# Optimization experiments

Measured on AMD Instinct MI355X. Metric: run time of the kernel, lower is better.

The kernel has to match this reference:

```python
import jax, jax.numpy as jnp
import numpy as np

N, D, NUM_CLASSES = 4096, 1024, 10


def setup_inputs() -> dict:
    key = jax.random.key(0)
    k1, k2, k3 = jax.random.split(key, 3)
    return {
        "fm_s": jax.random.normal(k1, (N, D), dtype=jnp.float32),
        "fm_t": jax.random.normal(k2, (N, D), dtype=jnp.float32),
        "targets": jax.random.randint(k3, (N,), 0, NUM_CLASSES, dtype=jnp.int64),
        "fusion_true": 0,
    }


def reference(fm_s, fm_t, targets, fusion_true):
    # fusion_true == False branch of CL.forward (multi_index unused).
    # Pairwise squared distances ||s_i - t_j||^2 via the GEMM expansion
    # instead of materializing the [N, N, D] difference tensor.
    s2 = jnp.sum(fm_s * fm_s, axis=-1)            # [N]
    t2 = jnp.sum(fm_t * fm_t, axis=-1)            # [N]
    cross = jnp.einsum('id,jd->ij', fm_s, fm_t)   # [N, N]
    d2 = s2[:, None] + t2[None, :] - 2.0 * cross  # [N, N]

    # self_mask_pos[i, j] = 1 where targets[i] == targets[j]
    mask_pos = (targets[:, None] == targets[None, :]).astype(d2.dtype)  # [N, N]
    row_norm = jnp.sum(mask_pos, axis=-1, keepdims=True)                # [N, 1], >= 1

    loss_pos = d2 * mask_pos / row_norm           # [N, N]
    return jnp.mean(jnp.sum(loss_pos, axis=-1))   # scalar
```

## Files before the change

kernel.cpp:

```cpp
#include <hip/hip_runtime.h>

#define N_ROWS 4096
#define D_DIM  1024
#define NCLS   10

#define NSLICE     4
#define SLICE_W    (D_DIM / NSLICE)
#define CHUNK_ROWS 64
#define NCHUNK     (N_ROWS / CHUNK_ROWS)
#define NB2        (NCHUNK * NSLICE)
#define NB3        512

#define OFF_MEAN 0
#define OFF_PL   (NCLS * D_DIM)
#define OFF_PT2  (OFF_PL + NB3)
#define OFF_PT   (OFF_PT2 + NB2)
#define DET_FLOATS (OFF_PT + NCHUNK * NCLS * D_DIM)
#define ATOMIC_FLOATS OFF_PT

__global__ void k_partialT(const float* __restrict__ fm_t,
                           const int* __restrict__ tgt,
                           float* __restrict__ partialT,
                           float* __restrict__ pt2) {
    int chunk = blockIdx.x / NSLICE;
    int slice = blockIdx.x % NSLICE;
    int tid   = threadIdx.x;

    __shared__ int tl[CHUNK_ROWS];
    if (tid < CHUNK_ROWS) tl[tid] = tgt[chunk * CHUNK_ROWS + tid];
    __syncthreads();

    float acc[NCLS];
#pragma unroll
    for (int k = 0; k < NCLS; ++k) acc[k] = 0.f;
    float acc2 = 0.f;

    int col = slice * SLICE_W + tid;
    const float* base = fm_t + (size_t)chunk * CHUNK_ROWS * D_DIM + col;
#pragma unroll 4
    for (int r = 0; r < CHUNK_ROWS; ++r) {
        float v = base[(size_t)r * D_DIM];
        int   c = tl[r];
        acc2 += v * v;
#pragma unroll
        for (int k = 0; k < NCLS; ++k) acc[k] += (c == k) ? v : 0.f;
    }

    float* out = partialT + (size_t)chunk * NCLS * D_DIM + col;
#pragma unroll
    for (int k = 0; k < NCLS; ++k) out[k * D_DIM] = acc[k];

    __shared__ float red[256];
    red[tid] = acc2;
    __syncthreads();
    for (int s = 128; s > 0; s >>= 1) {
        if (tid < s) red[tid] += red[tid + s];
        __syncthreads();
    }
    if (tid == 0) pt2[blockIdx.x] = red[0];
}

__global__ void k_reduceT(const float* __restrict__ partialT,
                          const int* __restrict__ tgt,
                          float* __restrict__ meanT) {
    int tid = threadIdx.x;

    __shared__ int hist[NCLS];
    if (tid < NCLS) hist[tid] = 0;
    __syncthreads();
    for (int i = tid; i < N_ROWS; i += 256) atomicAdd(&hist[tgt[i]], 1);
    __syncthreads();

    int cell = blockIdx.x * 256 + tid;
    if (cell >= NCLS * D_DIM) return;
    float s = 0.f;
#pragma unroll 8
    for (int k = 0; k < NCHUNK; ++k)
        s += partialT[(size_t)k * NCLS * D_DIM + cell];
    meanT[cell] = s / (float)hist[cell / D_DIM];
}

__global__ void k_zero(float* __restrict__ p, int n) {
    int i = blockIdx.x * blockDim.x + threadIdx.x;
    if (i < n) p[i] = 0.f;
}

__global__ void k_partialT_atomic(const float* __restrict__ fm_t,
                                  const int* __restrict__ tgt,
                                  float* __restrict__ sumT,
                                  float* __restrict__ pt2) {
    int chunk = blockIdx.x / NSLICE;
    int slice = blockIdx.x % NSLICE;
    int tid   = threadIdx.x;

    __shared__ int tl[CHUNK_ROWS];
    if (tid < CHUNK_ROWS) tl[tid] = tgt[chunk * CHUNK_ROWS + tid];
    __syncthreads();

    float acc[NCLS];
#pragma unroll
    for (int k = 0; k < NCLS; ++k) acc[k] = 0.f;
    float acc2 = 0.f;

    int col = slice * SLICE_W + tid;
    const float* base = fm_t + (size_t)chunk * CHUNK_ROWS * D_DIM + col;
    for (int r = 0; r < CHUNK_ROWS; ++r) {
        float v = base[(size_t)r * D_DIM];
        int   c = tl[r];
        acc2 += v * v;
#pragma unroll
        for (int k = 0; k < NCLS; ++k) acc[k] += (c == k) ? v : 0.f;
    }
#pragma unroll
    for (int k = 0; k < NCLS; ++k) atomicAdd(&sumT[k * D_DIM + col], acc[k]);

    __shared__ float red[256];
    red[tid] = acc2;
    __syncthreads();
    for (int s = 128; s > 0; s >>= 1) {
        if (tid < s) red[tid] += red[tid + s];
        __syncthreads();
    }
    if (tid == 0) pt2[blockIdx.x] = red[0];
}

__global__ void k_divmean(float* __restrict__ meanT, const int* __restrict__ tgt) {
    int tid = threadIdx.x;
    __shared__ int hist[NCLS];
    if (tid < NCLS) hist[tid] = 0;
    __syncthreads();
    for (int i = tid; i < N_ROWS; i += 256) atomicAdd(&hist[tgt[i]], 1);
    __syncthreads();
    int cell = blockIdx.x * 256 + tid;
    if (cell >= NCLS * D_DIM) return;
    meanT[cell] = meanT[cell] / (float)hist[cell / D_DIM];
}

__global__ void k_main(const float* __restrict__ fm_s,
                       const int* __restrict__ tgt,
                       const float* __restrict__ meanT,
                       float* __restrict__ partialLoss) {
    int tid = threadIdx.x;
    int bid = blockIdx.x;
    float acc = 0.f;

    const int ROWS_PER_BLK = N_ROWS / NB3;
#pragma unroll
    for (int r = 0; r < ROWS_PER_BLK; ++r) {
        int row = bid * ROWS_PER_BLK + r;
        int c   = tgt[row];
        const float4* s4 = (const float4*)(fm_s + (size_t)row * D_DIM);
        const float4* m4 = (const float4*)(meanT + (size_t)c * D_DIM);
        float4 sv = s4[tid];
        float4 mv = m4[tid];
        acc += sv.x * sv.x + sv.y * sv.y + sv.z * sv.z + sv.w * sv.w
             - 2.f * (sv.x * mv.x + sv.y * mv.y + sv.z * mv.z + sv.w * mv.w);
    }

    __shared__ float red[256];
    red[tid] = acc;
    __syncthreads();
    for (int s = 128; s > 0; s >>= 1) {
        if (tid < s) red[tid] += red[tid + s];
        __syncthreads();
    }
    if (tid == 0) partialLoss[bid] = red[0];
}

__global__ void k_final(const float* __restrict__ partialLoss,
                        const float* __restrict__ pt2,
                        float* __restrict__ out) {
    int tid = threadIdx.x;
    double acc = 0.0;
    for (int i = tid; i < NB3; i += 256) acc += (double)partialLoss[i];
    acc += (double)pt2[tid];
    __shared__ double red[256];
    red[tid] = acc;
    __syncthreads();
    for (int s = 128; s > 0; s >>= 1) {
        if (tid < s) red[tid] += red[tid + s];
        __syncthreads();
    }
    if (tid == 0) out[0] = (float)(red[0] / (double)N_ROWS);
}

extern "C" void kernel_launch(void* const* d_in, const int* in_sizes, int n_in,
                              void* d_out, int out_size, void* d_ws, size_t ws_size,
                              hipStream_t stream) {
    const float* fm_s = (const float*)d_in[0];
    const float* fm_t = (const float*)d_in[1];
    const int*   tgt  = (const int*)d_in[2];

    float* ws       = (float*)d_ws;
    float* meanT    = ws + OFF_MEAN;
    float* ploss    = ws + OFF_PL;
    float* pt2      = ws + OFF_PT2;
    float* partialT = ws + OFF_PT;
    float* outp     = (float*)d_out;

    if (ws_size >= (size_t)DET_FLOATS * sizeof(float)) {
        k_partialT<<<NB2, 256, 0, stream>>>(fm_t, tgt, partialT, pt2);
        k_reduceT<<<(NCLS * D_DIM + 255) / 256, 256, 0, stream>>>(partialT, tgt, meanT);
    } else {
        k_zero<<<(NCLS * D_DIM + 255) / 256, 256, 0, stream>>>(meanT, NCLS * D_DIM);
        k_partialT_atomic<<<NB2, 256, 0, stream>>>(fm_t, tgt, meanT, pt2);
        k_divmean<<<(NCLS * D_DIM + 255) / 256, 256, 0, stream>>>(meanT, tgt);
    }

    k_main<<<NB3, 256, 0, stream>>>(fm_s, tgt, meanT, ploss);
    k_final<<<1, 256, 0, stream>>>(ploss, pt2, outp);
}
```

Measured before the change: 28.92 us.

## Compute loss from per-class sums of both matrices in two kernels

Restructures the computation so that both fm_s and fm_t are reduced into per-class column sums in a single pass, and the cross term becomes a dot product of the class sums divided by class counts. The per-row k_main pass over fm_s and the separate final kernel are removed. A last-block atomic counter in pass 2 performs the final reduction, cutting the launch count from four to two. The change adds a larger partial-sum workspace and a threadfence/counter protocol, and class dispatch uses a wave-uniform switch via readfirstlane.

```diff
diff --git a/kernel.cpp b/kernel.cpp
--- a/kernel.cpp
+++ b/kernel.cpp
@@ -4,51 +4,80 @@
 #define D_DIM  1024
 #define NCLS   10
 
-#define NSLICE     4
-#define SLICE_W    (D_DIM / NSLICE)
-#define CHUNK_ROWS 64
-#define NCHUNK     (N_ROWS / CHUNK_ROWS)
-#define NB2        (NCHUNK * NSLICE)
-#define NB3        512
-
-#define OFF_MEAN 0
-#define OFF_PL   (NCLS * D_DIM)
-#define OFF_PT2  (OFF_PL + NB3)
-#define OFF_PT   (OFF_PT2 + NB2)
-#define DET_FLOATS (OFF_PT + NCHUNK * NCLS * D_DIM)
-#define ATOMIC_FLOATS OFF_PT
-
-__global__ void k_partialT(const float* __restrict__ fm_t,
-                           const int* __restrict__ tgt,
-                           float* __restrict__ partialT,
-                           float* __restrict__ pt2) {
-    int chunk = blockIdx.x / NSLICE;
-    int slice = blockIdx.x % NSLICE;
-    int tid   = threadIdx.x;
-
-    __shared__ int tl[CHUNK_ROWS];
-    if (tid < CHUNK_ROWS) tl[tid] = tgt[chunk * CHUNK_ROWS + tid];
-    __syncthreads();
-
-    float acc[NCLS];
-#pragma unroll
-    for (int k = 0; k < NCLS; ++k) acc[k] = 0.f;
+
+#define CHUNK     32
+#define NCHUNK    (N_ROWS / CHUNK)
+#define SLICE_W   512
+#define NSLICE    (D_DIM / SLICE_W)
+#define K1_BLOCKS (2 * NSLICE * NCHUNK)
+#define K2_BLOCKS 40
+#define CS        (NCLS * SLICE_W)
+
+#define OFF_CTR   0
+#define OFF_ACC2  16
+#define OFF_DOTP  (OFF_ACC2 + K1_BLOCKS)
+#define OFF_PART  544
+#define PART_FLOATS (NSLICE * NCHUNK * NCLS * SLICE_W)
+#define NEED_FLOATS (OFF_PART + 2 * PART_FLOATS)
+
+#define OFF_FBS   544
+#define FB_FLOATS (OFF_FBS + 2 * NCLS * D_DIM)
+
+__global__ __launch_bounds__(256) void k_pass1(const float* __restrict__ fm_s,
+                                               const float* __restrict__ fm_t,
+                                               const int* __restrict__ tgt,
+                                               float* __restrict__ ws) {
+    const int bid = blockIdx.x, tid = threadIdx.x;
+    const int mat   = bid >> 8;
+    const int rem   = bid & 255;
+    const int slice = rem >> 7;
+    const int chunk = rem & 127;
+
+    if (bid == 0 && tid == 0) ((int*)ws)[OFF_CTR] = 0;
+
+    __shared__ int tl[CHUNK];
+    if (tid < CHUNK) tl[tid] = tgt[chunk * CHUNK + tid];
+    __syncthreads();
+
+    const float* src  = mat ? fm_t : fm_s;
+    const float* base = src + (size_t)chunk * CHUNK * D_DIM + slice * SLICE_W + tid * 2;
+
+    float2 a[NCLS];
+#pragma unroll
+    for (int k = 0; k < NCLS; ++k) a[k] = make_float2(0.f, 0.f);
     float acc2 = 0.f;
 
-    int col = slice * SLICE_W + tid;
-    const float* base = fm_t + (size_t)chunk * CHUNK_ROWS * D_DIM + col;
-#pragma unroll 4
-    for (int r = 0; r < CHUNK_ROWS; ++r) {
-        float v = base[(size_t)r * D_DIM];
-        int   c = tl[r];
-        acc2 += v * v;
-#pragma unroll
-        for (int k = 0; k < NCLS; ++k) acc[k] += (c == k) ? v : 0.f;
-    }
-
-    float* out = partialT + (size_t)chunk * NCLS * D_DIM + col;
-#pragma unroll
-    for (int k = 0; k < NCLS; ++k) out[k * D_DIM] = acc[k];
+#pragma unroll
+    for (int r0 = 0; r0 < CHUNK; r0 += 16) {
+        float2 v[16];
+#pragma unroll
+        for (int j = 0; j < 16; ++j)
+            v[j] = *(const float2*)(base + (size_t)(r0 + j) * D_DIM);
+#pragma unroll
+        for (int j = 0; j < 16; ++j) {
+            const float x = v[j].x, y = v[j].y;
+            acc2 += x * x + y * y;
+            const int c = __builtin_amdgcn_readfirstlane(tl[r0 + j]);
+            switch (c) {
+                case 0: a[0].x += x; a[0].y += y; break;
+                case 1: a[1].x += x; a[1].y += y; break;
+                case 2: a[2].x += x; a[2].y += y; break;
+                case 3: a[3].x += x; a[3].y += y; break;
+                case 4: a[4].x += x; a[4].y += y; break;
+                case 5: a[5].x += x; a[5].y += y; break;
+                case 6: a[6].x += x; a[6].y += y; break;
+                case 7: a[7].x += x; a[7].y += y; break;
+                case 8: a[8].x += x; a[8].y += y; break;
+                default: a[9].x += x; a[9].y += y; break;
+            }
+        }
+    }
+
+    float* part = ws + OFF_PART + (size_t)mat * PART_FLOATS
+                + (size_t)(slice * NCHUNK + chunk) * CS + tid * 2;
+#pragma unroll
+    for (int k = 0; k < NCLS; ++k)
+        *(float2*)(part + (size_t)k * SLICE_W) = a[k];
 
     __shared__ float red[256];
     red[tid] = acc2;
@@ -57,13 +86,79 @@
         if (tid < s) red[tid] += red[tid + s];
         __syncthreads();
     }
-    if (tid == 0) pt2[blockIdx.x] = red[0];
-}
-
-__global__ void k_reduceT(const float* __restrict__ partialT,
-                          const int* __restrict__ tgt,
-                          float* __restrict__ meanT) {
-    int tid = threadIdx.x;
+    if (tid == 0) ws[OFF_ACC2 + bid] = red[0];
+}
+
+__global__ __launch_bounds__(256) void k_pass2(const int* __restrict__ tgt,
+                                               float* __restrict__ ws,
+                                               float* __restrict__ out) {
+    const int b = blockIdx.x, tid = threadIdx.x;
+    const int cls  = b >> 2;
+    const int colq = b & 3;
+    const int g    = tid >> 6;
+    const int ct   = tid & 63;
+    const int mat  = g >> 1;
+    const int half = g & 1;
+    const int slice = colq >> 1;
+    const int c512  = (colq & 1) * 256 + ct * 4;
+
+    const float* p = ws + OFF_PART + (size_t)mat * PART_FLOATS
+                   + (size_t)slice * ((size_t)NCHUNK * CS)
+                   + (size_t)(half * 64) * CS
+                   + (size_t)cls * SLICE_W + c512;
+
+    float4 s0 = {0,0,0,0}, s1 = {0,0,0,0}, s2 = {0,0,0,0}, s3 = {0,0,0,0};
+#pragma unroll
+    for (int c0 = 0; c0 < 64; c0 += 16) {
+        float4 v[16];
+#pragma unroll
+        for (int j = 0; j < 16; ++j)
+            v[j] = *(const float4*)(p + (size_t)(c0 + j) * CS);
+#pragma unroll
+        for (int j = 0; j < 16; ++j) {
+            float4& acc = ((j & 3) == 0) ? s0 : ((j & 3) == 1) ? s1 : ((j & 3) == 2) ? s2 : s3;
+            acc.x += v[j].x; acc.y += v[j].y; acc.z += v[j].z; acc.w += v[j].w;
+        }
+    }
+    float4 sum;
+    sum.x = (s0.x + s1.x) + (s2.x + s3.x);
+    sum.y = (s0.y + s1.y) + (s2.y + s3.y);
+    sum.z = (s0.z + s1.z) + (s2.z + s3.z);
+    sum.w = (s0.w + s1.w) + (s2.w + s3.w);
+
+    __shared__ float4 red4[4][64];
+    red4[g][ct] = sum;
+    __syncthreads();
+
+    __shared__ float prodRed[64];
+    if (tid < 64) {
+        float4 A, B;
+        A.x = red4[0][tid].x + red4[1][tid].x;
+        A.y = red4[0][tid].y + red4[1][tid].y;
+        A.z = red4[0][tid].z + red4[1][tid].z;
+        A.w = red4[0][tid].w + red4[1][tid].w;
+        B.x = red4[2][tid].x + red4[3][tid].x;
+        B.y = red4[2][tid].y + red4[3][tid].y;
+        B.z = red4[2][tid].z + red4[3][tid].z;
+        B.w = red4[2][tid].w + red4[3][tid].w;
+        prodRed[tid] = A.x * B.x + A.y * B.y + A.z * B.z + A.w * B.w;
+    }
+    __syncthreads();
+    for (int s = 32; s > 0; s >>= 1) {
+        if (tid < s) prodRed[tid] += prodRed[tid + s];
+        __syncthreads();
+    }
+
+    __shared__ int isLast;
+    if (tid == 0) {
+        ws[OFF_DOTP + b] = prodRed[0];
+        __threadfence();
+        int old = atomicAdd((int*)ws + OFF_CTR, 1);
+        isLast = (old == K2_BLOCKS - 1) ? 1 : 0;
+    }
+    __syncthreads();
+    if (!isLast) return;
+    __threadfence();
 
     __shared__ int hist[NCLS];
     if (tid < NCLS) hist[tid] = 0;
@@ -71,48 +166,73 @@
     for (int i = tid; i < N_ROWS; i += 256) atomicAdd(&hist[tgt[i]], 1);
     __syncthreads();
 
-    int cell = blockIdx.x * 256 + tid;
-    if (cell >= NCLS * D_DIM) return;
-    float s = 0.f;
-#pragma unroll 8
-    for (int k = 0; k < NCHUNK; ++k)
-        s += partialT[(size_t)k * NCLS * D_DIM + cell];
-    meanT[cell] = s / (float)hist[cell / D_DIM];
-}
-
-__global__ void k_zero(float* __restrict__ p, int n) {
-    int i = blockIdx.x * blockDim.x + threadIdx.x;
-    if (i < n) p[i] = 0.f;
-}
-
-__global__ void k_partialT_atomic(const float* __restrict__ fm_t,
-                                  const int* __restrict__ tgt,
-                                  float* __restrict__ sumT,
-                                  float* __restrict__ pt2) {
-    int chunk = blockIdx.x / NSLICE;
-    int slice = blockIdx.x % NSLICE;
-    int tid   = threadIdx.x;
-
-    __shared__ int tl[CHUNK_ROWS];
-    if (tid < CHUNK_ROWS) tl[tid] = tgt[chunk * CHUNK_ROWS + tid];
-    __syncthreads();
-
-    float acc[NCLS];
-#pragma unroll
-    for (int k = 0; k < NCLS; ++k) acc[k] = 0.f;
+    double v = (double)ws[OFF_ACC2 + tid] + (double)ws[OFF_ACC2 + tid + 256];
+    if (tid < K2_BLOCKS) {
+        int n = hist[tid >> 2];
+        if (n > 0) v -= 2.0 * (double)ws[OFF_DOTP + tid] / (double)n;
+    }
+    __shared__ double dred[256];
+    dred[tid] = v;
+    __syncthreads();
+    for (int s = 128; s > 0; s >>= 1) {
+        if (tid < s) dred[tid] += dred[tid + s];
+        __syncthreads();
+    }
+    if (tid == 0) out[0] = (float)(dred[0] / (double)N_ROWS);
+}
+
+__global__ void k_fb_zero(float* __restrict__ ws) {
+    int i = blockIdx.x * 256 + threadIdx.x;
+    if (i < 2 * NCLS * D_DIM) ws[OFF_FBS + i] = 0.f;
+}
+
+__global__ __launch_bounds__(256) void k_fb_acc(const float* __restrict__ fm_s,
+                                                const float* __restrict__ fm_t,
+                                                const int* __restrict__ tgt,
+                                                float* __restrict__ ws) {
+    const int bid = blockIdx.x, tid = threadIdx.x;
+    const int mat   = bid >> 8;
+    const int rem   = bid & 255;
+    const int slice = rem >> 7;
+    const int chunk = rem & 127;
+
+    __shared__ int tl[CHUNK];
+    if (tid < CHUNK) tl[tid] = tgt[chunk * CHUNK + tid];
+    __syncthreads();
+
+    const float* src  = mat ? fm_t : fm_s;
+    const float* base = src + (size_t)chunk * CHUNK * D_DIM + slice * SLICE_W + tid * 2;
+
+    float2 a[NCLS];
+#pragma unroll
+    for (int k = 0; k < NCLS; ++k) a[k] = make_float2(0.f, 0.f);
     float acc2 = 0.f;
 
-    int col = slice * SLICE_W + tid;
-    const float* base = fm_t + (size_t)chunk * CHUNK_ROWS * D_DIM + col;
-    for (int r = 0; r < CHUNK_ROWS; ++r) {
-        float v = base[(size_t)r * D_DIM];
-        int   c = tl[r];
-        acc2 += v * v;
-#pragma unroll
-        for (int k = 0; k < NCLS; ++k) acc[k] += (c == k) ? v : 0.f;
-    }
-#pragma unroll
-    for (int k = 0; k < NCLS; ++k) atomicAdd(&sumT[k * D_DIM + col], acc[k]);
+    for (int r = 0; r < CHUNK; ++r) {
+        float2 v = *(const float2*)(base + (size_t)r * D_DIM);
+        acc2 += v.x * v.x + v.y * v.y;
+        const int c = __builtin_amdgcn_readfirstlane(tl[r]);
+        switch (c) {
+            case 0: a[0].x += v.x; a[0].y += v.y; break;
+            case 1: a[1].x += v.x; a[1].y += v.y; break;
+            case 2: a[2].x += v.x; a[2].y += v.y; break;
+            case 3: a[3].x += v.x; a[3].y += v.y; break;
+            case 4: a[4].x += v.x; a[4].y += v.y; break;
+            case 5: a[5].x += v.x; a[5].y += v.y; break;
+            case 6: a[6].x += v.x; a[6].y += v.y; break;
+            case 7: a[7].x += v.x; a[7].y += v.y; break;
+            case 8: a[8].x += v.x; a[8].y += v.y; break;
+            default: a[9].x += v.x; a[9].y += v.y; break;
+        }
+    }
+
+    int col = slice * SLICE_W + tid * 2;
+    float* dst = ws + OFF_FBS + (size_t)mat * NCLS * D_DIM + col;
+#pragma unroll
+    for (int k = 0; k < NCLS; ++k) {
+        atomicAdd(dst + (size_t)k * D_DIM,     a[k].x);
+        atomicAdd(dst + (size_t)k * D_DIM + 1, a[k].y);
+    }
 
     __shared__ float red[256];
     red[tid] = acc2;
@@ -121,67 +241,36 @@
         if (tid < s) red[tid] += red[tid + s];
         __syncthreads();
     }
-    if (tid == 0) pt2[blockIdx.x] = red[0];
-}
-
-__global__ void k_divmean(float* __restrict__ meanT, const int* __restrict__ tgt) {
-    int tid = threadIdx.x;
+    if (tid == 0) ws[OFF_ACC2 + bid] = red[0];
+}
+
+__global__ __launch_bounds__(256) void k_fb_fin(const int* __restrict__ tgt,
+                                                float* __restrict__ ws,
+                                                float* __restrict__ out) {
+    const int tid = threadIdx.x;
     __shared__ int hist[NCLS];
     if (tid < NCLS) hist[tid] = 0;
     __syncthreads();
     for (int i = tid; i < N_ROWS; i += 256) atomicAdd(&hist[tgt[i]], 1);
     __syncthreads();
-    int cell = blockIdx.x * 256 + tid;
-    if (cell >= NCLS * D_DIM) return;
-    meanT[cell] = meanT[cell] / (float)hist[cell / D_DIM];
-}
-
-__global__ void k_main(const float* __restrict__ fm_s,
-                       const int* __restrict__ tgt,
-                       const float* __restrict__ meanT,
-                       float* __restrict__ partialLoss) {
-    int tid = threadIdx.x;
-    int bid = blockIdx.x;
-    float acc = 0.f;
-
-    const int ROWS_PER_BLK = N_ROWS / NB3;
-#pragma unroll
-    for (int r = 0; r < ROWS_PER_BLK; ++r) {
-        int row = bid * ROWS_PER_BLK + r;
-        int c   = tgt[row];
-        const float4* s4 = (const float4*)(fm_s + (size_t)row * D_DIM);
-        const float4* m4 = (const float4*)(meanT + (size_t)c * D_DIM);
-        float4 sv = s4[tid];
-        float4 mv = m4[tid];
-        acc += sv.x * sv.x + sv.y * sv.y + sv.z * sv.z + sv.w * sv.w
-             - 2.f * (sv.x * mv.x + sv.y * mv.y + sv.z * mv.z + sv.w * mv.w);
-    }
-
-    __shared__ float red[256];
-    red[tid] = acc;
-    __syncthreads();
-    for (int s = 128; s > 0; s >>= 1) {
-        if (tid < s) red[tid] += red[tid + s];
-        __syncthreads();
-    }
-    if (tid == 0) partialLoss[bid] = red[0];
-}
-
-__global__ void k_final(const float* __restrict__ partialLoss,
-                        const float* __restrict__ pt2,
-                        float* __restrict__ out) {
-    int tid = threadIdx.x;
-    double acc = 0.0;
-    for (int i = tid; i < NB3; i += 256) acc += (double)partialLoss[i];
-    acc += (double)pt2[tid];
-    __shared__ double red[256];
-    red[tid] = acc;
-    __syncthreads();
-    for (int s = 128; s > 0; s >>= 1) {
-        if (tid < s) red[tid] += red[tid + s];
-        __syncthreads();
-    }
-    if (tid == 0) out[0] = (float)(red[0] / (double)N_ROWS);
+
+    double v = (double)ws[OFF_ACC2 + tid] + (double)ws[OFF_ACC2 + tid + 256];
+    for (int i = tid; i < NCLS * D_DIM; i += 256) {
+        int n = hist[i >> 10];
+        if (n > 0) {
+            double sS = ws[OFF_FBS + i];
+            double sT = ws[OFF_FBS + NCLS * D_DIM + i];
+            v -= 2.0 * sS * sT / (double)n;
+        }
+    }
+    __shared__ double dred[256];
+    dred[tid] = v;
+    __syncthreads();
+    for (int s = 128; s > 0; s >>= 1) {
+        if (tid < s) dred[tid] += dred[tid + s];
+        __syncthreads();
+    }
+    if (tid == 0) out[0] = (float)(dred[0] / (double)N_ROWS);
 }
 
 extern "C" void kernel_launch(void* const* d_in, const int* in_sizes, int n_in,
@@ -191,22 +280,15 @@
     const float* fm_t = (const float*)d_in[1];
     const int*   tgt  = (const int*)d_in[2];
 
-    float* ws       = (float*)d_ws;
-    float* meanT    = ws + OFF_MEAN;
-    float* ploss    = ws + OFF_PL;
-    float* pt2      = ws + OFF_PT2;
-    float* partialT = ws + OFF_PT;
-    float* outp     = (float*)d_out;
-
-    if (ws_size >= (size_t)DET_FLOATS * sizeof(float)) {
-        k_partialT<<<NB2, 256, 0, stream>>>(fm_t, tgt, partialT, pt2);
-        k_reduceT<<<(NCLS * D_DIM + 255) / 256, 256, 0, stream>>>(partialT, tgt, meanT);
+    float* ws   = (float*)d_ws;
+    float* outp = (float*)d_out;
+
+    if (ws_size >= (size_t)NEED_FLOATS * sizeof(float)) {
+        k_pass1<<<K1_BLOCKS, 256, 0, stream>>>(fm_s, fm_t, tgt, ws);
+        k_pass2<<<K2_BLOCKS, 256, 0, stream>>>(tgt, ws, outp);
     } else {
-        k_zero<<<(NCLS * D_DIM + 255) / 256, 256, 0, stream>>>(meanT, NCLS * D_DIM);
-        k_partialT_atomic<<<NB2, 256, 0, stream>>>(fm_t, tgt, meanT, pt2);
-        k_divmean<<<(NCLS * D_DIM + 255) / 256, 256, 0, stream>>>(meanT, tgt);
-    }
-
-    k_main<<<NB3, 256, 0, stream>>>(fm_s, tgt, meanT, ploss);
-    k_final<<<1, 256, 0, stream>>>(ploss, pt2, outp);
-}
+        k_fb_zero<<<(2 * NCLS * D_DIM + 255) / 256, 256, 0, stream>>>(ws);
+        k_fb_acc<<<K1_BLOCKS, 256, 0, stream>>>(fm_s, fm_t, tgt, ws);
+        k_fb_fin<<<1, 256, 0, stream>>>(tgt, ws, outp);
+    }
+}
```

Measured after the change: 29.73 us. 2.8% more time.
